# Optimization experiments

Measured on AMD Instinct MI355X. Metric: run time of the kernel, lower is better.

Reference implementation:

```python
import jax, jax.numpy as jnp
import numpy as np
import math

FS, N_FFT, NUM_BANDS, NUM_BINS = 16000, 512, 31, 257
H = 96  # dim_hidden

def band_partition():
    f_min, f_max = FS / N_FFT, FS / 2.0
    z_min = 69.0 + 12.0 * math.log2(f_min / 440.0)
    z_max = 69.0 + 12.0 * math.log2(f_max / 440.0)
    z = np.linspace(z_min, z_max, NUM_BANDS + 2)
    f_points = 440.0 * 2.0 ** ((z - 69.0) / 12.0)
    bins = np.round(f_points * N_FFT / FS).astype(np.int64)
    bins[0] = 0
    bands = []
    for i in range(NUM_BANDS):
        s = max(0, int(bins[i]))
        e = min(NUM_BINS, int(bins[i + 2]) + 1)
        if e <= s:
            e = s + 1
        bands.append((s, e))
    return bands

BANDS = band_partition()

def hann(L):
    # torch.hann_window default (periodic=True)
    return 0.5 - 0.5 * jnp.cos(2.0 * jnp.pi * jnp.arange(L, dtype=jnp.float32) / L)

def chan_ln(x, eps=1e-5):
    # AdaNorm2d assumed = LayerNorm over channel dim, no affine
    m = jnp.mean(x, axis=1, keepdims=True)
    v = jnp.var(x, axis=1, keepdims=True)
    return (x - m) * jax.lax.rsqrt(v + eps)

def prelu(x, a):
    return jnp.where(x >= 0, x, a * x)

def setup_inputs() -> dict:
    key = jax.random.key(0)
    ks = jax.random.split(key, 20)
    B, T = 4, 1000
    return {
        'mix_repr': jax.random.normal(ks[0], (B, H, NUM_BINS, T), jnp.float32),
        'spin': jax.random.normal(ks[1], (B, 64, NUM_BINS, T), jnp.float32),
        'doa': jax.random.normal(ks[2], (B, 36), jnp.float32),
        'enc_w': jax.random.normal(ks[3], (NUM_BANDS, H, 64), jnp.float32) * 0.05,
        'enc_b': jax.random.normal(ks[4], (NUM_BANDS, H), jnp.float32) * 0.05,
        'enc_a': 0.25 * jnp.ones((NUM_BANDS,), jnp.float32),
        'dqg_w': jax.random.normal(ks[5], (NUM_BANDS, 2 * H, 36), jnp.float32) * 0.05,
        'dqg_b': jax.random.normal(ks[6], (NUM_BANDS, 2 * H), jnp.float32) * 0.05,
        'dec_w': jax.random.normal(ks[7], (NUM_BANDS, H, H), jnp.float32) * 0.05,
        'dec_b': jax.random.normal(ks[8], (NUM_BANDS, H), jnp.float32) * 0.05,
        'dec_a': 0.25 * jnp.ones((NUM_BANDS,), jnp.float32),
        'qw': jax.random.normal(ks[9], (H, H), jnp.float32) * 0.05,
        'qb': jax.random.normal(ks[10], (H,), jnp.float32) * 0.05,
        'kw': jax.random.normal(ks[11], (H, H), jnp.float32) * 0.05,
        'kb': jax.random.normal(ks[12], (H,), jnp.float32) * 0.05,
        'vw': jax.random.normal(ks[13], (H, H), jnp.float32) * 0.05,
        'vb': jax.random.normal(ks[14], (H,), jnp.float32) * 0.05,
        'ow': jax.random.normal(ks[15], (H, H), jnp.float32) * 0.05,
        'ob': jax.random.normal(ks[16], (H,), jnp.float32) * 0.05,
    }

def reference(mix_repr, spin, doa, enc_w, enc_b, enc_a, dqg_w, dqg_b,
              dec_w, dec_b, dec_a, qw, qb, kw, kb, vw, vb, ow, ob):
    B, D, F, T = mix_repr.shape
    merged = jnp.zeros((B, H, F, T), mix_repr.dtype)
    wsum = jnp.zeros((F,), mix_repr.dtype)
    for k, (s, e) in enumerate(BANDS):  # fixed set of 31 static ragged bands
        L = e - s
        win = hann(L)
        sub = spin[:, :, s:e, :]                                   # [B,64,L,T]
        feat = jnp.einsum('oc,bcft->boft', enc_w[k], sub) + enc_b[k][None, :, None, None]
        feat = prelu(chan_ln(feat), enc_a[k])
        qp = doa @ dqg_w[k].T + dqg_b[k]                           # [B,2H]
        gamma, beta = qp[:, :H], qp[:, H:]
        tgt = (1.0 + gamma)[:, :, None, None] * feat + beta[:, :, None, None]
        dec = jnp.einsum('oc,bcft->boft', dec_w[k], tgt) + dec_b[k][None, :, None, None]
        dec = prelu(chan_ln(dec), dec_a[k])
        merged = merged.at[:, :, s:e, :].add(dec * win[None, None, :, None])
        wsum = wsum.at[s:e].add(win)
    merged = merged / jnp.clip(wsum, 1e-8)[None, None, :, None]
    # MixtureQueryFusion: 1x1 conv cross-attention gate
    Q = jnp.einsum('oc,bcft->boft', qw, mix_repr) + qb[None, :, None, None]
    K = jnp.einsum('oc,bcft->boft', kw, merged) + kb[None, :, None, None]
    V = jnp.einsum('oc,bcft->boft', vw, merged) + vb[None, :, None, None]
    attn = jax.nn.sigmoid(jnp.sum(Q * K, axis=1, keepdims=True) / jnp.sqrt(jnp.float32(H)))
    attended = V * attn
    out = mix_repr + jnp.einsum('oc,bcft->boft', ow, attended) + ob[None, :, None, None]
    return out
```

## Files before the change

### kernel.cpp

```cpp
#include <hip/hip_runtime.h>
#include <math.h>

#define NBANDS 31
#define FT 257000

typedef __attribute__((ext_vector_type(8))) short bh8;
typedef __attribute__((ext_vector_type(4))) float f4;
typedef __attribute__((ext_vector_type(4))) float f4v;

__constant__ int d_bs[NBANDS] = {0,1,1,2,2,2,3,3,4,5,6,7,8,10,11,13,16,19,23,27,32,38,45,54,64,76,91,108,128,152,181};
__constant__ int d_be[NBANDS] = {2,3,3,3,4,4,5,6,7,8,9,11,12,14,17,20,24,28,33,39,46,55,65,77,92,109,129,153,182,216,257};

__device__ __forceinline__ unsigned short b16u(float v) {
  __bf16 h = (__bf16)v;
  return __builtin_bit_cast(unsigned short, h);
}
__device__ __forceinline__ unsigned pk2(float a, float b) {
  return (unsigned)b16u(a) | ((unsigned)b16u(b) << 16);
}
__device__ __forceinline__ float hann1(int i, int L) {
  return 0.5f - 0.5f * cosf(6.283185307179586f * (float)i / (float)L);
}

__global__ __launch_bounds__(256) void prep_w(
    const float* __restrict__ enc_w, const float* __restrict__ dec_w,
    const float* __restrict__ qw, const float* __restrict__ kw,
    const float* __restrict__ vw, const float* __restrict__ ow,
    unsigned short* __restrict__ w16) {
  const int stride = gridDim.x * blockDim.x;
  for (int i = blockIdx.x * blockDim.x + threadIdx.x; i < 513024; i += stride) {
    float v;
    if (i < 190464) {
      const int k = i / 6144, r = i - k * 6144;
      const int tile = r >> 9, li = r & 511;
      const int lane = li >> 3, j = li & 7;
      const int g = lane >> 4, n = lane & 15;
      const int mt = tile >> 1, kt = tile & 1;
      v = enc_w[k * 6144 + (mt * 16 + n) * 64 + kt * 32 + g * 8 + j];
    } else if (i < 476160) {
      const int i2 = i - 190464;
      const int k = i2 / 9216, r = i2 - k * 9216;
      const int tile = r >> 9, li = r & 511;
      const int lane = li >> 3, j = li & 7;
      const int g = lane >> 4, n = lane & 15;
      const int mt = tile / 3, kt = tile - mt * 3;
      v = dec_w[k * 9216 + (mt * 16 + n) * 96 + kt * 32 + g * 8 + j];
    } else {
      const int i2 = i - 476160;
      const int a = i2 / 9216, r = i2 - a * 9216;
      const int tile = r >> 9, li = r & 511;
      const int lane = li >> 3, j = li & 7;
      const int g = lane >> 4, n = lane & 15;
      const int mt = tile / 3, kt = tile - mt * 3;
      const float* src = (a == 0) ? qw : (a == 1) ? kw : (a == 2) ? vw : ow;
      v = src[(mt * 16 + n) * 96 + kt * 32 + g * 8 + j];
    }
    w16[i] = b16u(v);
  }
}

__global__ __launch_bounds__(192) void qp_kernel(const float* __restrict__ doa,
                                                 const float* __restrict__ dqg_w,
                                                 const float* __restrict__ dqg_b,
                                                 float* __restrict__ gbuf) {
  const int k = blockIdx.x, b = blockIdx.y;
  const int tid = threadIdx.x;
  __shared__ float sdoa[36];
  if (tid < 36) sdoa[tid] = doa[b * 36 + tid];
  __syncthreads();
  const float* wr = dqg_w + (k * 192 + tid) * 36;
  float acc = dqg_b[k * 192 + tid];
  #pragma unroll
  for (int i = 0; i < 36; ++i) acc = fmaf(wr[i], sdoa[i], acc);
  if (tid < 96) acc += 1.0f;
  gbuf[(k * 4 + b) * 192 + tid] = acc;
}

__global__ __launch_bounds__(96) void prep_dec(
    const float* __restrict__ dec_w, const float* __restrict__ dec_b,
    const float* __restrict__ gbuf,
    unsigned short* __restrict__ dec16b, float* __restrict__ decBb) {
  const int k = blockIdx.x, b = blockIdx.y;
  const int o = threadIdx.x;
  __shared__ float gm[96], bt[96];
  gm[o] = gbuf[(k * 4 + b) * 192 + o];
  bt[o] = gbuf[(k * 4 + b) * 192 + 96 + o];
  __syncthreads();
  const float* wr = dec_w + k * 9216 + o * 96;
  float bias = dec_b[k * 96 + o];
  unsigned short* dst = dec16b + (b * 31 + k) * 9216;
  const int mt = o >> 4, n = o & 15;
  for (int c = 0; c < 96; ++c) {
    const float wv = wr[c];
    bias = fmaf(wv, bt[c], bias);
    const int kt = c >> 5, g = (c & 31) >> 3, j = c & 7;
    dst[((mt * 3 + kt) << 9) + (((g << 4) + n) << 3) + j] = b16u(wv * gm[c]);
  }
  decBb[(b * 31 + k) * 96 + o] = bias;
}

__global__ __launch_bounds__(320) void tab_kernel(float* __restrict__ ftab) {
  const int f = blockIdx.x * blockDim.x + threadIdx.x;
  if (f >= 257) return;
  int k0 = 0; while (d_be[k0] <= f) ++k0;
  int k1 = k0; while (k1 < NBANDS && d_bs[k1] <= f) ++k1;
  float wsum = 0.f, wn[5];
  for (int k = k0; k < k1; ++k) {
    const float wv = hann1(f - d_bs[k], d_be[k] - d_bs[k]);
    wn[k - k0] = wv; wsum += wv;
  }
  float* o = ftab + f * 8;
  o[0] = (float)k0; o[1] = (float)(k1 - k0); o[2] = 1.0f / fmaxf(wsum, 1e-8f);
  #pragma unroll
  for (int j = 0; j < 5; ++j) o[3 + j] = (j < k1 - k0) ? wn[j] : 0.f;
}

#define LDSWAIT asm volatile("s_waitcnt lgkmcnt(0)" ::: "memory")

__device__ __forceinline__ void init6(f4* acc, const float* s, int off) {
  #pragma unroll
  for (int mt = 0; mt < 6; ++mt) {
    const float4 bb = *reinterpret_cast<const float4*>(s + mt * 16 + off);
    acc[mt] = (f4){bb.x, bb.y, bb.z, bb.w};
  }
}
__device__ __forceinline__ void ln96(const f4* acc, float& mean, float& rs) {
  float s0 = 0.f, s1 = 0.f, s2 = 0.f, s3 = 0.f;
  float q0 = 0.f, q1 = 0.f, q2 = 0.f, q3 = 0.f;
  #pragma unroll
  for (int mt = 0; mt < 6; ++mt) {
    const float a0 = acc[mt][0], a1 = acc[mt][1], a2 = acc[mt][2], a3 = acc[mt][3];
    s0 += a0; s1 += a1; s2 += a2; s3 += a3;
    q0 = fmaf(a0, a0, q0); q1 = fmaf(a1, a1, q1);
    q2 = fmaf(a2, a2, q2); q3 = fmaf(a3, a3, q3);
  }
  float sm = (s0 + s1) + (s2 + s3);
  float sq = (q0 + q1) + (q2 + q3);
  sm += __shfl_xor(sm, 16); sm += __shfl_xor(sm, 32);
  sq += __shfl_xor(sq, 16); sq += __shfl_xor(sq, 32);
  mean = sm * (1.f / 96.f);
  rs = rsqrtf(sq * (1.f / 96.f) - mean * mean + 1e-5f);
}
__device__ __forceinline__ void load6s(bh8* dst, const unsigned short* p, int step9) {
  #pragma unroll
  for (int mt = 0; mt < 6; ++mt)
    dst[mt] = *reinterpret_cast<const bh8*>(p + ((mt * step9) << 9));
}

__global__ __launch_bounds__(256, 3) void fused_mfma(
    const float* __restrict__ mix, const float* __restrict__ spin,
    const unsigned short* __restrict__ enc16, const float* __restrict__ enc_b, const float* __restrict__ enc_a,
    const unsigned short* __restrict__ dec16b, const float* __restrict__ decBb, const float* __restrict__ dec_a,
    const float* __restrict__ ftab,
    const unsigned short* __restrict__ q16, const float* __restrict__ qb,
    const unsigned short* __restrict__ k16, const float* __restrict__ kb,
    const unsigned short* __restrict__ v16, const float* __restrict__ vb,
    const unsigned short* __restrict__ o16, const float* __restrict__ ob,
    float* __restrict__ out) {
  const int id0 = (int)blockIdx.x;
  const int id  = (id0 & 7) * 2056 + (id0 >> 3);
  const int tt  = id & 15;
  const int fb  = id >> 4;
  const int f   = fb % 257;
  const int b   = fb / 257;
  const int t0  = tt << 6;

  const int tid  = threadIdx.x;
  const int lane = tid & 63;
  const int w    = tid >> 6;
  const int g    = lane >> 4;
  const int n    = lane & 15;
  const int col  = (w << 4) + n;
  const int t    = t0 + col;
  const int tcl  = (t < 1000) ? t : 999;
  const int sw   = (n & 7) << 3;
  const int lb   = lane << 3;
  const int bk   = b * 31;

  __shared__ __align__(16) char smem[26112];
  unsigned short* XT = (unsigned short*)smem;
  float* stage = (float*)(smem + 16384);
  float* OS = (float*)smem;
  unsigned short* xw = XT + col * 128;

  const float* ft = ftab + f * 8;
  const int k0 = (int)ft[0];
  const int nb = (int)ft[1];
  const float winv = ft[2];

  {
    const int tot = (nb << 8) + 384;
    for (int i = tid; i < tot; i += 256) {
      const int kk = i >> 8, r = i & 255;
      float v = 0.f;
      if (kk < nb) {
        const int k = k0 + kk;
        if      (r < 96)  v = enc_b[k * 96 + r];
        else if (r < 192) v = decBb[(bk + k) * 96 + (r - 96)];
        else if (r == 192) v = enc_a[k];
        else if (r == 193) v = dec_a[k];
        else if (r == 194) v = ft[3 + kk];
      } else {
        const int r2 = i - (nb << 8);
        v = (r2 < 96) ? qb[r2] : (r2 < 192) ? kb[r2 - 96] : (r2 < 288) ? vb[r2 - 192] : ob[r2 - 288];
      }
      stage[i] = v;
    }
  }

  const float* spL = spin + b * 64 * FT + f * 1000 + tcl;
  const float* mxL = mix  + b * 96 * FT + f * 1000 + tcl;

  bh8 spb[2];
  {
    float spf[16];
    #pragma unroll
    for (int j = 0; j < 8; ++j) spf[j]     = __builtin_nontemporal_load(spL + (g * 8 + j) * FT);
    #pragma unroll
    for (int j = 0; j < 8; ++j) spf[8 + j] = __builtin_nontemporal_load(spL + (32 + g * 8 + j) * FT);
    #pragma unroll
    for (int kt = 0; kt < 2; ++kt)
      #pragma unroll
      for (int j = 0; j < 8; ++j) spb[kt][j] = (short)b16u(spf[kt * 8 + j]);
  }

  bh8 pre[6];
  load6s(pre, enc16 + k0 * 6144 + lb, 2);

  __syncthreads();

  f4 macc[6];
  #pragma unroll
  for (int mt = 0; mt < 6; ++mt) macc[mt] = (f4){0.f, 0.f, 0.f, 0.f};

  const int oo = g * 4;

  for (int kk = 0; kk < nb; ++kk) {
    const int k = k0 + kk;
    const unsigned short* ew  = enc16 + k * 6144 + lb;
    const unsigned short* dwp = dec16b + (bk + k) * 9216 + lb;
    const float* stg = stage + (kk << 8);

    f4 acc[6];
    init6(acc, stg, oo);
    #pragma unroll
    for (int mt = 0; mt < 6; ++mt)
      acc[mt] = __builtin_amdgcn_mfma_f32_16x16x32_bf16(pre[mt], spb[0], acc[mt], 0, 0, 0);
    #pragma unroll
    for (int mt = 0; mt < 6; ++mt) {
      const bh8 af = *reinterpret_cast<const bh8*>(ew + ((mt * 2 + 1) << 9));
      acc[mt] = __builtin_amdgcn_mfma_f32_16x16x32_bf16(af, spb[1], acc[mt], 0, 0, 0);
    }

    load6s(pre, dwp, 3);

    float mean, rs;
    ln96(acc, mean, rs);
    const float ea = stg[192];
    #pragma unroll
    for (int mt = 0; mt < 6; ++mt) {
      float x0 = (acc[mt][0] - mean) * rs; x0 = (x0 >= 0.f) ? x0 : ea * x0;
      float x1 = (acc[mt][1] - mean) * rs; x1 = (x1 >= 0.f) ? x1 : ea * x1;
      float x2 = (acc[mt][2] - mean) * rs; x2 = (x2 >= 0.f) ? x2 : ea * x2;
      float x3 = (acc[mt][3] - mean) * rs; x3 = (x3 >= 0.f) ? x3 : ea * x3;
      uint2 u;
      u.x = pk2(x0, x1);
      u.y = pk2(x2, x3);
      *reinterpret_cast<uint2*>(xw + ((mt * 16 + oo) ^ sw)) = u;
    }
    LDSWAIT;

    f4 dacc[6];
    init6(dacc, stg + 96, oo);
    {
      const bh8 bf0 = *reinterpret_cast<const bh8*>(xw + ((0 * 32 + g * 8) ^ sw));
      #pragma unroll
      for (int mt = 0; mt < 6; ++mt)
        dacc[mt] = __builtin_amdgcn_mfma_f32_16x16x32_bf16(pre[mt], bf0, dacc[mt], 0, 0, 0);
    }

    {
      const bool more = (kk + 1 < nb);
      load6s(pre, more ? (enc16 + (k + 1) * 6144 + lb) : (q16 + lb), more ? 2 : 3);
    }

    #pragma unroll
    for (int kt = 1; kt < 3; ++kt) {
      const bh8 bf = *reinterpret_cast<const bh8*>(xw + ((kt * 32 + g * 8) ^ sw));
      #pragma unroll
      for (int mt = 0; mt < 6; ++mt) {
        const bh8 af = *reinterpret_cast<const bh8*>(dwp + ((mt * 3 + kt) << 9));
        dacc[mt] = __builtin_amdgcn_mfma_f32_16x16x32_bf16(af, bf, dacc[mt], 0, 0, 0);
      }
    }
    float mean2, rs2;
    ln96(dacc, mean2, rs2);
    const float da = stg[193];
    const float win = stg[194];
    #pragma unroll
    for (int mt = 0; mt < 6; ++mt)
      #pragma unroll
      for (int r = 0; r < 4; ++r) {
        float x = (dacc[mt][r] - mean2) * rs2;
        x = (x >= 0.f) ? x : da * x;
        macc[mt][r] = fmaf(win, x, macc[mt][r]);
      }
  }

  float mxf[24];
  #pragma unroll
  for (int kt = 0; kt < 3; ++kt)
    #pragma unroll
    for (int j = 0; j < 8; ++j) mxf[kt * 8 + j] = mxL[(kt * 32 + g * 8 + j) * FT];

  #pragma unroll
  for (int mt = 0; mt < 6; ++mt) {
    uint2 u;
    u.x = pk2(macc[mt][0] * winv, macc[mt][1] * winv);
    u.y = pk2(macc[mt][2] * winv, macc[mt][3] * winv);
    *reinterpret_cast<uint2*>(xw + ((mt * 16 + oo) ^ sw)) = u;
  }
  LDSWAIT;
  bh8 gfr[3];
  #pragma unroll
  for (int kt = 0; kt < 3; ++kt) gfr[kt] = *reinterpret_cast<const bh8*>(xw + ((kt * 32 + g * 8) ^ sw));

  bh8 mxb[3];
  #pragma unroll
  for (int kt = 0; kt < 3; ++kt)
    #pragma unroll
    for (int j = 0; j < 8; ++j) mxb[kt][j] = (short)b16u(mxf[kt * 8 + j]);

  const float* stQ = stage + (nb << 8);

  f4 qacc[6];
  init6(qacc, stQ, oo);
  const unsigned short* qp16 = q16 + lb;
  #pragma unroll
  for (int mt = 0; mt < 6; ++mt)
    qacc[mt] = __builtin_amdgcn_mfma_f32_16x16x32_bf16(pre[mt], mxb[0], qacc[mt], 0, 0, 0);
  load6s(pre, k16 + lb, 3);
  #pragma unroll
  for (int kt = 1; kt < 3; ++kt)
    #pragma unroll
    for (int mt = 0; mt < 6; ++mt) {
      const bh8 af = *reinterpret_cast<const bh8*>(qp16 + ((mt * 3 + kt) << 9));
      qacc[mt] = __builtin_amdgcn_mfma_f32_16x16x32_bf16(af, mxb[kt], qacc[mt], 0, 0, 0);
    }
  f4 kacc[6];
  init6(kacc, stQ + 96, oo);
  const unsigned short* kp16 = k16 + lb;
  #pragma unroll
  for (int mt = 0; mt < 6; ++mt)
    kacc[mt] = __builtin_amdgcn_mfma_f32_16x16x32_bf16(pre[mt], gfr[0], kacc[mt], 0, 0, 0);
  load6s(pre, v16 + lb, 3);
  #pragma unroll
  for (int kt = 1; kt < 3; ++kt)
    #pragma unroll
    for (int mt = 0; mt < 6; ++mt) {
      const bh8 af = *reinterpret_cast<const bh8*>(kp16 + ((mt * 3 + kt) << 9));
      kacc[mt] = __builtin_amdgcn_mfma_f32_16x16x32_bf16(af, gfr[kt], kacc[mt], 0, 0, 0);
    }
  float p0 = 0.f, p1 = 0.f;
  #pragma unroll
  for (int mt = 0; mt < 6; ++mt) {
    p0 = fmaf(qacc[mt][0], kacc[mt][0], p0);
    p1 = fmaf(qacc[mt][1], kacc[mt][1], p1);
    p0 = fmaf(qacc[mt][2], kacc[mt][2], p0);
    p1 = fmaf(qacc[mt][3], kacc[mt][3], p1);
  }
  float p = p0 + p1;
  p += __shfl_xor(p, 16); p += __shfl_xor(p, 32);
  const float sig = 1.f / (1.f + __expf(-p * 0.10206207261596575f));

  f4 vacc[6];
  init6(vacc, stQ + 192, oo);
  const unsigned short* vp16 = v16 + lb;
  #pragma unroll
  for (int mt = 0; mt < 6; ++mt)
    vacc[mt] = __builtin_amdgcn_mfma_f32_16x16x32_bf16(pre[mt], gfr[0], vacc[mt], 0, 0, 0);
  load6s(pre, o16 + lb, 3);
  #pragma unroll
  for (int kt = 1; kt < 3; ++kt)
    #pragma unroll
    for (int mt = 0; mt < 6; ++mt) {
      const bh8 af = *reinterpret_cast<const bh8*>(vp16 + ((mt * 3 + kt) << 9));
      vacc[mt] = __builtin_amdgcn_mfma_f32_16x16x32_bf16(af, gfr[kt], vacc[mt], 0, 0, 0);
    }
  #pragma unroll
  for (int mt = 0; mt < 6; ++mt) {
    uint2 u;
    u.x = pk2(vacc[mt][0] * sig, vacc[mt][1] * sig);
    u.y = pk2(vacc[mt][2] * sig, vacc[mt][3] * sig);
    *reinterpret_cast<uint2*>(xw + ((mt * 16 + oo) ^ sw)) = u;
  }
  LDSWAIT;
  bh8 afr[3];
  #pragma unroll
  for (int kt = 0; kt < 3; ++kt) afr[kt] = *reinterpret_cast<const bh8*>(xw + ((kt * 32 + g * 8) ^ sw));

  f4 oacc[6];
  init6(oacc, stQ + 288, oo);
  const unsigned short* op16 = o16 + lb;
  #pragma unroll
  for (int mt = 0; mt < 6; ++mt)
    oacc[mt] = __builtin_amdgcn_mfma_f32_16x16x32_bf16(pre[mt], afr[0], oacc[mt], 0, 0, 0);
  #pragma unroll
  for (int kt = 1; kt < 3; ++kt)
    #pragma unroll
    for (int mt = 0; mt < 6; ++mt) {
      const bh8 af = *reinterpret_cast<const bh8*>(op16 + ((mt * 3 + kt) << 9));
      oacc[mt] = __builtin_amdgcn_mfma_f32_16x16x32_bf16(af, afr[kt], oacc[mt], 0, 0, 0);
    }

  __syncthreads();

  #pragma unroll
  for (int mt = 0; mt < 6; ++mt)
    #pragma unroll
    for (int r = 0; r < 4; ++r)
      OS[(mt * 16 + oo + r) * 68 + col] = oacc[mt][r];

  __syncthreads();

  const int cvalid = 1000 - t0;
  if (cvalid >= 64) {
    #pragma unroll
    for (int it = 0; it < 6; ++it) {
      const int i   = it * 256 + tid;
      const int row = i >> 4;
      const int c4  = (i & 15) << 2;
      f4v v = *reinterpret_cast<const f4v*>(&OS[row * 68 + c4]);
      const long gi = (long)(b * 96 + row) * FT + f * 1000 + t0 + c4;
      const f4v m = *reinterpret_cast<const f4v*>(mix + gi);
      v = v + m;
      __builtin_nontemporal_store(v, reinterpret_cast<f4v*>(out + gi));
    }
  } else {
    #pragma unroll
    for (int it = 0; it < 24; ++it) {
      const int i   = it * 256 + tid;
      const int row = i >> 6;
      const int c   = i & 63;
      if (c < cvalid) {
        const long gi = (long)(b * 96 + row) * FT + f * 1000 + t0 + c;
        __builtin_nontemporal_store(OS[row * 68 + c] + mix[gi], out + gi);
      }
    }
  }
}

extern "C" void kernel_launch(void* const* d_in, const int* in_sizes, int n_in,
                              void* d_out, int out_size, void* d_ws, size_t ws_size,
                              hipStream_t stream) {
  (void)in_sizes; (void)n_in; (void)out_size; (void)ws_size;
  const float* mix   = (const float*)d_in[0];
  const float* spin  = (const float*)d_in[1];
  const float* doa   = (const float*)d_in[2];
  const float* enc_w = (const float*)d_in[3];
  const float* enc_b = (const float*)d_in[4];
  const float* enc_a = (const float*)d_in[5];
  const float* dqg_w = (const float*)d_in[6];
  const float* dqg_b = (const float*)d_in[7];
  const float* dec_w = (const float*)d_in[8];
  const float* dec_b = (const float*)d_in[9];
  const float* dec_a = (const float*)d_in[10];
  const float* qw    = (const float*)d_in[11];
  const float* qb    = (const float*)d_in[12];
  const float* kw    = (const float*)d_in[13];
  const float* kb    = (const float*)d_in[14];
  const float* vw    = (const float*)d_in[15];
  const float* vb    = (const float*)d_in[16];
  const float* oww   = (const float*)d_in[17];
  const float* obb   = (const float*)d_in[18];
  float* outp = (float*)d_out;

  unsigned short* w16 = (unsigned short*)d_ws;
  unsigned short* enc16 = w16;
  unsigned short* q16   = w16 + 476160;
  unsigned short* k16   = q16 + 9216;
  unsigned short* v16   = k16 + 9216;
  unsigned short* o16   = v16 + 9216;
  float* gbws = (float*)((char*)d_ws + 1026048);
  float* ftab = (float*)((char*)d_ws + 1121280);
  unsigned short* dec16b = (unsigned short*)((char*)d_ws + 1129504);
  float* decBb = (float*)((char*)d_ws + 3415072);

  hipLaunchKernelGGL(prep_w, dim3(512), dim3(256), 0, stream,
                     enc_w, dec_w, qw, kw, vw, oww, w16);
  hipLaunchKernelGGL(qp_kernel, dim3(NBANDS, 4), dim3(192), 0, stream,
                     doa, dqg_w, dqg_b, gbws);
  hipLaunchKernelGGL(prep_dec, dim3(NBANDS, 4), dim3(96), 0, stream,
                     dec_w, dec_b, gbws, dec16b, decBb);
  hipLaunchKernelGGL(tab_kernel, dim3(1), dim3(320), 0, stream, ftab);
  hipLaunchKernelGGL(fused_mfma, dim3(16448), dim3(256), 0, stream,
                     mix, spin, enc16, enc_b, enc_a, dec16b, decBb, dec_a, ftab,
                     q16, qb, k16, kb, v16, vb, o16, obb, outp);
}
```

Measured before the change: 545.3 us.

## Split fused kernel into band encoder/decoder and QKVO gate kernels

```diff
diff --git a/kernel.cpp b/kernel.cpp
--- a/kernel.cpp
+++ b/kernel.cpp
@@ -116,6 +116,8 @@
 }
 
 #define LDSWAIT asm volatile("s_waitcnt lgkmcnt(0)" ::: "memory")
+#define PRIO1 __builtin_amdgcn_s_setprio(1)
+#define PRIO0 __builtin_amdgcn_s_setprio(0)
 
 __device__ __forceinline__ void init6(f4* acc, const float* s, int off) {
   #pragma unroll
@@ -123,6 +125,10 @@
     const float4 bb = *reinterpret_cast<const float4*>(s + mt * 16 + off);
     acc[mt] = (f4){bb.x, bb.y, bb.z, bb.w};
   }
+}
+__device__ __forceinline__ f4 init1(const float* s, int mt, int off) {
+  const float4 bb = *reinterpret_cast<const float4*>(s + mt * 16 + off);
+  return (f4){bb.x, bb.y, bb.z, bb.w};
 }
 __device__ __forceinline__ void ln96(const f4* acc, float& mean, float& rs) {
   float s0 = 0.f, s1 = 0.f, s2 = 0.f, s3 = 0.f;
@@ -145,6 +151,338 @@
   #pragma unroll
   for (int mt = 0; mt < 6; ++mt)
     dst[mt] = *reinterpret_cast<const bh8*>(p + ((mt * step9) << 9));
+}
+
+__global__ __launch_bounds__(256, 4) void band_mfma(
+    const float* __restrict__ spin,
+    const unsigned short* __restrict__ enc16, const float* __restrict__ enc_b, const float* __restrict__ enc_a,
+    const unsigned short* __restrict__ dec16b, const float* __restrict__ decBb, const float* __restrict__ dec_a,
+    const float* __restrict__ ftab,
+    bh8* __restrict__ gout) {
+  const int id0 = (int)blockIdx.x;
+  const int id  = (id0 & 7) * 2056 + (id0 >> 3);
+  const int tt  = id & 15;
+  const int fb  = id >> 4;
+  const int f   = fb % 257;
+  const int b   = fb / 257;
+  const int t0  = tt << 6;
+
+  const int tid  = threadIdx.x;
+  const int lane = tid & 63;
+  const int w    = tid >> 6;
+  const int g    = lane >> 4;
+  const int n    = lane & 15;
+  const int col  = (w << 4) + n;
+  const int t    = t0 + col;
+  const int tcl  = (t < 1000) ? t : 999;
+  const int sw   = (n & 7) << 3;
+  const int lb   = lane << 3;
+  const int bk   = b * 31;
+
+  __shared__ __align__(16) unsigned short XT[64 * 128];
+  __shared__ __align__(16) float stage[5 * 256];
+  unsigned short* xw = XT + col * 128;
+
+  const float* ft = ftab + f * 8;
+  const int k0 = (int)ft[0];
+  const int nb = (int)ft[1];
+  const float winv = ft[2];
+
+  {
+    const int tot = nb << 8;
+    for (int i = tid; i < tot; i += 256) {
+      const int kk = i >> 8, r = i & 255;
+      const int k = k0 + kk;
+      float v = 0.f;
+      if      (r < 96)  v = enc_b[k * 96 + r];
+      else if (r < 192) v = decBb[(bk + k) * 96 + (r - 96)];
+      else if (r == 192) v = enc_a[k];
+      else if (r == 193) v = dec_a[k];
+      else if (r == 194) v = ft[3 + kk];
+      stage[i] = v;
+    }
+  }
+
+  const float* spL = spin + b * 64 * FT + f * 1000 + tcl;
+
+  bh8 spb[2];
+  {
+    float spf[16];
+    #pragma unroll
+    for (int j = 0; j < 8; ++j) spf[j]     = __builtin_nontemporal_load(spL + (g * 8 + j) * FT);
+    #pragma unroll
+    for (int j = 0; j < 8; ++j) spf[8 + j] = __builtin_nontemporal_load(spL + (32 + g * 8 + j) * FT);
+    #pragma unroll
+    for (int kt = 0; kt < 2; ++kt)
+      #pragma unroll
+      for (int j = 0; j < 8; ++j) spb[kt][j] = (short)b16u(spf[kt * 8 + j]);
+  }
+
+  bh8 pre[6];
+  load6s(pre, enc16 + k0 * 6144 + lb, 2);
+
+  __syncthreads();
+
+  f4 macc[6];
+  #pragma unroll
+  for (int mt = 0; mt < 6; ++mt) macc[mt] = (f4){0.f, 0.f, 0.f, 0.f};
+
+  const int oo = g * 4;
+
+  for (int kk = 0; kk < nb; ++kk) {
+    const int k = k0 + kk;
+    const unsigned short* ew  = enc16 + k * 6144 + lb;
+    const unsigned short* dwp = dec16b + (bk + k) * 9216 + lb;
+    const float* stg = stage + (kk << 8);
+
+    f4 acc[6];
+    init6(acc, stg, oo);
+    PRIO1;
+    #pragma unroll
+    for (int mt = 0; mt < 6; ++mt)
+      acc[mt] = __builtin_amdgcn_mfma_f32_16x16x32_bf16(pre[mt], spb[0], acc[mt], 0, 0, 0);
+    #pragma unroll
+    for (int mt = 0; mt < 6; ++mt) {
+      const bh8 af = *reinterpret_cast<const bh8*>(ew + ((mt * 2 + 1) << 9));
+      acc[mt] = __builtin_amdgcn_mfma_f32_16x16x32_bf16(af, spb[1], acc[mt], 0, 0, 0);
+    }
+    PRIO0;
+
+    load6s(pre, dwp, 3);
+
+    float mean, rs;
+    ln96(acc, mean, rs);
+    const float ea = stg[192];
+    #pragma unroll
+    for (int mt = 0; mt < 6; ++mt) {
+      float x0 = (acc[mt][0] - mean) * rs; x0 = (x0 >= 0.f) ? x0 : ea * x0;
+      float x1 = (acc[mt][1] - mean) * rs; x1 = (x1 >= 0.f) ? x1 : ea * x1;
+      float x2 = (acc[mt][2] - mean) * rs; x2 = (x2 >= 0.f) ? x2 : ea * x2;
+      float x3 = (acc[mt][3] - mean) * rs; x3 = (x3 >= 0.f) ? x3 : ea * x3;
+      uint2 u;
+      u.x = pk2(x0, x1);
+      u.y = pk2(x2, x3);
+      *reinterpret_cast<uint2*>(xw + ((mt * 16 + oo) ^ sw)) = u;
+    }
+    LDSWAIT;
+
+    f4 dacc[6];
+    init6(dacc, stg + 96, oo);
+    PRIO1;
+    {
+      const bh8 bf0 = *reinterpret_cast<const bh8*>(xw + ((0 * 32 + g * 8) ^ sw));
+      #pragma unroll
+      for (int mt = 0; mt < 6; ++mt)
+        dacc[mt] = __builtin_amdgcn_mfma_f32_16x16x32_bf16(pre[mt], bf0, dacc[mt], 0, 0, 0);
+    }
+    PRIO0;
+
+    {
+      const bool more = (kk + 1 < nb);
+      if (more) load6s(pre, enc16 + (k + 1) * 6144 + lb, 2);
+    }
+
+    PRIO1;
+    #pragma unroll
+    for (int kt = 1; kt < 3; ++kt) {
+      const bh8 bf = *reinterpret_cast<const bh8*>(xw + ((kt * 32 + g * 8) ^ sw));
+      #pragma unroll
+      for (int mt = 0; mt < 6; ++mt) {
+        const bh8 af = *reinterpret_cast<const bh8*>(dwp + ((mt * 3 + kt) << 9));
+        dacc[mt] = __builtin_amdgcn_mfma_f32_16x16x32_bf16(af, bf, dacc[mt], 0, 0, 0);
+      }
+    }
+    PRIO0;
+    float mean2, rs2;
+    ln96(dacc, mean2, rs2);
+    const float da = stg[193];
+    const float win = stg[194];
+    #pragma unroll
+    for (int mt = 0; mt < 6; ++mt)
+      #pragma unroll
+      for (int r = 0; r < 4; ++r) {
+        float x = (dacc[mt][r] - mean2) * rs2;
+        x = (x >= 0.f) ? x : da * x;
+        macc[mt][r] = fmaf(win, x, macc[mt][r]);
+      }
+  }
+
+  #pragma unroll
+  for (int mt = 0; mt < 6; ++mt) {
+    uint2 u;
+    u.x = pk2(macc[mt][0] * winv, macc[mt][1] * winv);
+    u.y = pk2(macc[mt][2] * winv, macc[mt][3] * winv);
+    *reinterpret_cast<uint2*>(xw + ((mt * 16 + oo) ^ sw)) = u;
+  }
+  LDSWAIT;
+  bh8* gw = gout + (long)id * 768 + w * 192 + lane;
+  #pragma unroll
+  for (int kt = 0; kt < 3; ++kt) {
+    const bh8 gfr = *reinterpret_cast<const bh8*>(xw + ((kt * 32 + g * 8) ^ sw));
+    gw[kt * 64] = gfr;
+  }
+}
+
+__global__ __launch_bounds__(256, 5) void qkvo_mfma(
+    const float* __restrict__ mix, const bh8* __restrict__ gin,
+    const unsigned short* __restrict__ q16, const float* __restrict__ qb,
+    const unsigned short* __restrict__ k16, const float* __restrict__ kb,
+    const unsigned short* __restrict__ v16, const float* __restrict__ vb,
+    const unsigned short* __restrict__ o16, const float* __restrict__ ob,
+    float* __restrict__ out) {
+  const int id0 = (int)blockIdx.x;
+  const int id  = (id0 & 7) * 2056 + (id0 >> 3);
+  const int tt  = id & 15;
+  const int fb  = id >> 4;
+  const int f   = fb % 257;
+  const int b   = fb / 257;
+  const int t0  = tt << 6;
+
+  const int tid  = threadIdx.x;
+  const int lane = tid & 63;
+  const int w    = tid >> 6;
+  const int g    = lane >> 4;
+  const int n    = lane & 15;
+  const int col  = (w << 4) + n;
+  const int t    = t0 + col;
+  const int tcl  = (t < 1000) ? t : 999;
+  const int sw   = (n & 7) << 3;
+  const int lb   = lane << 3;
+
+  __shared__ __align__(16) char smem[27648];
+  unsigned short* XT = (unsigned short*)smem;
+  float* stage = (float*)(smem + 26112);
+  float* OS = (float*)smem;
+  unsigned short* xw = XT + col * 128;
+
+  for (int i = tid; i < 384; i += 256) {
+    float v = (i < 96) ? qb[i] : (i < 192) ? kb[i - 96] : (i < 288) ? vb[i - 192] : ob[i - 288];
+    stage[i] = v;
+  }
+
+  const float* mxL = mix + b * 96 * FT + f * 1000 + tcl;
+
+  bh8 gfr[3];
+  {
+    const bh8* gr = gin + (long)id * 768 + w * 192 + lane;
+    #pragma unroll
+    for (int kt = 0; kt < 3; ++kt) gfr[kt] = gr[kt * 64];
+  }
+
+  bh8 mxb[3];
+  {
+    float mxf[24];
+    #pragma unroll
+    for (int kt = 0; kt < 3; ++kt)
+      #pragma unroll
+      for (int j = 0; j < 8; ++j) mxf[kt * 8 + j] = mxL[(kt * 32 + g * 8 + j) * FT];
+    #pragma unroll
+    for (int kt = 0; kt < 3; ++kt)
+      #pragma unroll
+      for (int j = 0; j < 8; ++j) mxb[kt][j] = (short)b16u(mxf[kt * 8 + j]);
+  }
+
+  __syncthreads();
+
+  const int oo = g * 4;
+  const unsigned short* qp16 = q16 + lb;
+  const unsigned short* kp16 = k16 + lb;
+  const unsigned short* vp16 = v16 + lb;
+  const unsigned short* op16 = o16 + lb;
+
+  float p0 = 0.f, p1 = 0.f;
+  #pragma unroll
+  for (int mt = 0; mt < 6; ++mt) {
+    f4 qa = init1(stage, mt, oo);
+    f4 ka = init1(stage + 96, mt, oo);
+    PRIO1;
+    #pragma unroll
+    for (int kt = 0; kt < 3; ++kt) {
+      const bh8 af = *reinterpret_cast<const bh8*>(qp16 + ((mt * 3 + kt) << 9));
+      qa = __builtin_amdgcn_mfma_f32_16x16x32_bf16(af, mxb[kt], qa, 0, 0, 0);
+    }
+    #pragma unroll
+    for (int kt = 0; kt < 3; ++kt) {
+      const bh8 af = *reinterpret_cast<const bh8*>(kp16 + ((mt * 3 + kt) << 9));
+      ka = __builtin_amdgcn_mfma_f32_16x16x32_bf16(af, gfr[kt], ka, 0, 0, 0);
+    }
+    PRIO0;
+    p0 = fmaf(qa[0], ka[0], p0);
+    p1 = fmaf(qa[1], ka[1], p1);
+    p0 = fmaf(qa[2], ka[2], p0);
+    p1 = fmaf(qa[3], ka[3], p1);
+  }
+  float p = p0 + p1;
+  p += __shfl_xor(p, 16); p += __shfl_xor(p, 32);
+  const float sig = 1.f / (1.f + __expf(-p * 0.10206207261596575f));
+
+  #pragma unroll
+  for (int mt = 0; mt < 6; ++mt) {
+    f4 va = init1(stage + 192, mt, oo);
+    PRIO1;
+    #pragma unroll
+    for (int kt = 0; kt < 3; ++kt) {
+      const bh8 af = *reinterpret_cast<const bh8*>(vp16 + ((mt * 3 + kt) << 9));
+      va = __builtin_amdgcn_mfma_f32_16x16x32_bf16(af, gfr[kt], va, 0, 0, 0);
+    }
+    PRIO0;
+    uint2 u;
+    u.x = pk2(va[0] * sig, va[1] * sig);
+    u.y = pk2(va[2] * sig, va[3] * sig);
+    *reinterpret_cast<uint2*>(xw + ((mt * 16 + oo) ^ sw)) = u;
+  }
+  LDSWAIT;
+  bh8 afr[3];
+  #pragma unroll
+  for (int kt = 0; kt < 3; ++kt) afr[kt] = *reinterpret_cast<const bh8*>(xw + ((kt * 32 + g * 8) ^ sw));
+
+  f4 oacc[6];
+  init6(oacc, stage + 288, oo);
+  PRIO1;
+  #pragma unroll
+  for (int kt = 0; kt < 3; ++kt)
+    #pragma unroll
+    for (int mt = 0; mt < 6; ++mt) {
+      const bh8 af = *reinterpret_cast<const bh8*>(op16 + ((mt * 3 + kt) << 9));
+      oacc[mt] = __builtin_amdgcn_mfma_f32_16x16x32_bf16(af, afr[kt], oacc[mt], 0, 0, 0);
+    }
+  PRIO0;
+
+  __syncthreads();
+
+  #pragma unroll
+  for (int mt = 0; mt < 6; ++mt)
+    #pragma unroll
+    for (int r = 0; r < 4; ++r)
+      OS[(mt * 16 + oo + r) * 68 + col] = oacc[mt][r];
+
+  __syncthreads();
+
+  const int cvalid = 1000 - t0;
+  if (cvalid >= 64) {
+    #pragma unroll
+    for (int it = 0; it < 6; ++it) {
+      const int i   = it * 256 + tid;
+      const int row = i >> 4;
+      const int c4  = (i & 15) << 2;
+      f4v v = *reinterpret_cast<const f4v*>(&OS[row * 68 + c4]);
+      const long gi = (long)(b * 96 + row) * FT + f * 1000 + t0 + c4;
+      const f4v m = *reinterpret_cast<const f4v*>(mix + gi);
+      v = v + m;
+      __builtin_nontemporal_store(v, reinterpret_cast<f4v*>(out + gi));
+    }
+  } else {
+    #pragma unroll
+    for (int it = 0; it < 24; ++it) {
+      const int i   = it * 256 + tid;
+      const int row = i >> 6;
+      const int c   = i & 63;
+      if (c < cvalid) {
+        const long gi = (long)(b * 96 + row) * FT + f * 1000 + t0 + c;
+        __builtin_nontemporal_store(OS[row * 68 + c] + mix[gi], out + gi);
+      }
+    }
+  }
 }
 
 __global__ __launch_bounds__(256, 3) void fused_mfma(
@@ -453,7 +791,7 @@
 extern "C" void kernel_launch(void* const* d_in, const int* in_sizes, int n_in,
                               void* d_out, int out_size, void* d_ws, size_t ws_size,
                               hipStream_t stream) {
-  (void)in_sizes; (void)n_in; (void)out_size; (void)ws_size;
+  (void)in_sizes; (void)n_in; (void)out_size;
   const float* mix   = (const float*)d_in[0];
   const float* spin  = (const float*)d_in[1];
   const float* doa   = (const float*)d_in[2];
@@ -485,6 +823,8 @@
   float* ftab = (float*)((char*)d_ws + 1121280);
   unsigned short* dec16b = (unsigned short*)((char*)d_ws + 1129504);
   float* decBb = (float*)((char*)d_ws + 3415072);
+  bh8* gfrag  = (bh8*)((char*)d_ws + 3462720);
+  const size_t need = 3462720ull + 202113024ull;
 
   hipLaunchKernelGGL(prep_w, dim3(512), dim3(256), 0, stream,
                      enc_w, dec_w, qw, kw, vw, oww, w16);
@@ -493,7 +833,15 @@
   hipLaunchKernelGGL(prep_dec, dim3(NBANDS, 4), dim3(96), 0, stream,
                      dec_w, dec_b, gbws, dec16b, decBb);
   hipLaunchKernelGGL(tab_kernel, dim3(1), dim3(320), 0, stream, ftab);
-  hipLaunchKernelGGL(fused_mfma, dim3(16448), dim3(256), 0, stream,
-                     mix, spin, enc16, enc_b, enc_a, dec16b, decBb, dec_a, ftab,
-                     q16, qb, k16, kb, v16, vb, o16, obb, outp);
-}
+
+  if (ws_size >= need) {
+    hipLaunchKernelGGL(band_mfma, dim3(16448), dim3(256), 0, stream,
+                       spin, enc16, enc_b, enc_a, dec16b, decBb, dec_a, ftab, gfrag);
+    hipLaunchKernelGGL(qkvo_mfma, dim3(16448), dim3(256), 0, stream,
+                       mix, gfrag, q16, qb, k16, kb, v16, vb, o16, obb, outp);
+  } else {
+    hipLaunchKernelGGL(fused_mfma, dim3(16448), dim3(256), 0, stream,
+                       mix, spin, enc16, enc_b, enc_a, dec16b, decBb, dec_a, ftab,
+                       q16, qb, k16, kb, v16, vb, o16, obb, outp);
+  }
+}
```

New measurement: 663.8 us. 21.7% more time.

## Software-pipeline encoder MFMA of next band with decoder LayerNorm epilogue

Applied to the files above, without the earlier changes.

```diff
diff --git a/kernel.cpp b/kernel.cpp
--- a/kernel.cpp
+++ b/kernel.cpp
@@ -235,14 +235,10 @@
 
   const int oo = g * 4;
 
-  for (int kk = 0; kk < nb; ++kk) {
-    const int k = k0 + kk;
-    const unsigned short* ew  = enc16 + k * 6144 + lb;
-    const unsigned short* dwp = dec16b + (bk + k) * 9216 + lb;
-    const float* stg = stage + (kk << 8);
-
-    f4 acc[6];
-    init6(acc, stg, oo);
+  f4 acc[6];
+  {
+    const unsigned short* ew = enc16 + k0 * 6144 + lb;
+    init6(acc, stage, oo);
     #pragma unroll
     for (int mt = 0; mt < 6; ++mt)
       acc[mt] = __builtin_amdgcn_mfma_f32_16x16x32_bf16(pre[mt], spb[0], acc[mt], 0, 0, 0);
@@ -251,8 +247,14 @@
       const bh8 af = *reinterpret_cast<const bh8*>(ew + ((mt * 2 + 1) << 9));
       acc[mt] = __builtin_amdgcn_mfma_f32_16x16x32_bf16(af, spb[1], acc[mt], 0, 0, 0);
     }
-
-    load6s(pre, dwp, 3);
+    load6s(pre, dec16b + (bk + k0) * 9216 + lb, 3);
+  }
+
+  for (int kk = 0; kk < nb; ++kk) {
+    const int k = k0 + kk;
+    const unsigned short* dwp = dec16b + (bk + k) * 9216 + lb;
+    const float* stg = stage + (kk << 8);
+    const bool more = (kk + 1 < nb);
 
     float mean, rs;
     ln96(acc, mean, rs);
@@ -278,11 +280,7 @@
       for (int mt = 0; mt < 6; ++mt)
         dacc[mt] = __builtin_amdgcn_mfma_f32_16x16x32_bf16(pre[mt], bf0, dacc[mt], 0, 0, 0);
     }
-
-    {
-      const bool more = (kk + 1 < nb);
-      load6s(pre, more ? (enc16 + (k + 1) * 6144 + lb) : (q16 + lb), more ? 2 : 3);
-    }
+    load6s(pre, more ? (enc16 + (k + 1) * 6144 + lb) : (q16 + lb), more ? 2 : 3);
 
     #pragma unroll
     for (int kt = 1; kt < 3; ++kt) {
@@ -293,18 +291,49 @@
         dacc[mt] = __builtin_amdgcn_mfma_f32_16x16x32_bf16(af, bf, dacc[mt], 0, 0, 0);
       }
     }
-    float mean2, rs2;
-    ln96(dacc, mean2, rs2);
-    const float da = stg[193];
-    const float win = stg[194];
-    #pragma unroll
-    for (int mt = 0; mt < 6; ++mt)
-      #pragma unroll
-      for (int r = 0; r < 4; ++r) {
-        float x = (dacc[mt][r] - mean2) * rs2;
-        x = (x >= 0.f) ? x : da * x;
-        macc[mt][r] = fmaf(win, x, macc[mt][r]);
+
+    if (more) {
+      const unsigned short* ew2 = enc16 + (k + 1) * 6144 + lb;
+      f4 acc2[6];
+      init6(acc2, stage + ((kk + 1) << 8), oo);
+      #pragma unroll
+      for (int mt = 0; mt < 6; ++mt)
+        acc2[mt] = __builtin_amdgcn_mfma_f32_16x16x32_bf16(pre[mt], spb[0], acc2[mt], 0, 0, 0);
+      #pragma unroll
+      for (int mt = 0; mt < 6; ++mt) {
+        const bh8 af = *reinterpret_cast<const bh8*>(ew2 + ((mt * 2 + 1) << 9));
+        acc2[mt] = __builtin_amdgcn_mfma_f32_16x16x32_bf16(af, spb[1], acc2[mt], 0, 0, 0);
       }
+      load6s(pre, dec16b + (bk + k + 1) * 9216 + lb, 3);
+
+      float mean2, rs2;
+      ln96(dacc, mean2, rs2);
+      const float da = stg[193];
+      const float win = stg[194];
+      #pragma unroll
+      for (int mt = 0; mt < 6; ++mt)
+        #pragma unroll
+        for (int r = 0; r < 4; ++r) {
+          float x = (dacc[mt][r] - mean2) * rs2;
+          x = (x >= 0.f) ? x : da * x;
+          macc[mt][r] = fmaf(win, x, macc[mt][r]);
+        }
+      #pragma unroll
+      for (int mt = 0; mt < 6; ++mt) acc[mt] = acc2[mt];
+    } else {
+      float mean2, rs2;
+      ln96(dacc, mean2, rs2);
+      const float da = stg[193];
+      const float win = stg[194];
+      #pragma unroll
+      for (int mt = 0; mt < 6; ++mt)
+        #pragma unroll
+        for (int r = 0; r < 4; ++r) {
+          float x = (dacc[mt][r] - mean2) * rs2;
+          x = (x >= 0.f) ? x : da * x;
+          macc[mt][r] = fmaf(win, x, macc[mt][r]);
+        }
+    }
   }
 
   float mxf[24];
```

Result: slower. 637.5 us (+16.9%).
